# Kernel tuning notes

Measured on AMD Instinct MI355X. Metric: run time of the kernel, lower is better.

The kernel has to match this reference:

```python
import jax, jax.numpy as jnp
import numpy as np

N = 50000
E = 250000
IN = 256
H = 4
D = 64  # h_feats // n_heads
C = 153


def setup_inputs() -> dict:
    key = jax.random.key(0)
    ks = jax.random.split(key, 32)
    def nrm(k, shape, scale=0.05):
        return jax.random.normal(k, shape, dtype=jnp.float32) * scale
    inp = {
        'x': nrm(ks[0], (N, IN), 1.0),
        'edge_index_a': jax.random.randint(ks[1], (2, E), 0, N, dtype=jnp.int32),
        'edge_index_b': jax.random.randint(ks[2], (2, E), 0, N, dtype=jnp.int32),
    }
    i = 3
    for layer in (0, 1):
        for et in ('a', 'b'):
            inp[f'W{layer}{et}'] = nrm(ks[i], (IN if layer == 0 else H * D, H * D)); i += 1
            inp[f'asrc{layer}{et}'] = nrm(ks[i], (H, D)); i += 1
            inp[f'adst{layer}{et}'] = nrm(ks[i], (H, D)); i += 1
            inp[f'b{layer}{et}'] = nrm(ks[i], (H * D,)); i += 1
    inp['Wout'] = nrm(ks[i], (H * D, C)); i += 1
    inp['bout'] = nrm(ks[i], (C,))
    return inp


def gat_conv(x, edge_index, W, a_src, a_dst, b):
    # PyG GATConv: shared linear, per-edge attention, dst-segmented softmax
    h = (x @ W).reshape(N, H, D)                 # [N, H, D]
    s_src = jnp.sum(h * a_src, axis=-1)          # [N, H]
    s_dst = jnp.sum(h * a_dst, axis=-1)          # [N, H]
    src, dst = edge_index[0], edge_index[1]
    e = jax.nn.leaky_relu(s_src[src] + s_dst[dst], negative_slope=0.2)  # [E, H]
    m = jax.ops.segment_max(e, dst, num_segments=N)                     # [N, H]
    m = jnp.where(jnp.isfinite(m), m, 0.0)       # isolated nodes -> 0
    p = jnp.exp(e - m[dst])                      # [E, H]
    z = jax.ops.segment_sum(p, dst, num_segments=N)
    alpha = p / (z[dst] + 1e-16)                 # [E, H]
    out = jax.ops.segment_sum(h[src] * alpha[:, :, None], dst, num_segments=N)
    return out.reshape(N, H * D) + b


def reference(x, edge_index_a, edge_index_b,
              W0a, asrc0a, adst0a, b0a, W0b, asrc0b, adst0b, b0b,
              W1a, asrc1a, adst1a, b1a, W1b, asrc1b, adst1b, b1b,
              Wout, bout):
    # layer 0: HeteroConv sums outputs of per-etype GATConvs
    h = gat_conv(x, edge_index_a, W0a, asrc0a, adst0a, b0a) + \
        gat_conv(x, edge_index_b, W0b, asrc0b, adst0b, b0b)
    h = jax.nn.leaky_relu(h, negative_slope=0.01)  # F.leaky_relu default; dropout is identity in eval
    # layer 1 (no activation after last layer)
    h = gat_conv(h, edge_index_a, W1a, asrc1a, adst1a, b1a) + \
        gat_conv(h, edge_index_b, W1b, asrc1b, adst1b, b1b)
    return h @ Wout + bout
```

## Files before the change

kernel.cpp:

```cpp
#include <hip/hip_runtime.h>
#include <math.h>

#define N_NODES 50000
#define E_EDGES 250000
#define HD 256
#define NH 4
#define DH 64
#define NC 153
#define KDIM 256
#define HD2 512
#define SLOTS 64

__device__ __forceinline__ unsigned short f2bf(float f) {
    unsigned u = __float_as_uint(f);
    u = u + 0x7FFFu + ((u >> 16) & 1u);
    return (unsigned short)(u >> 16);
}
__device__ __forceinline__ float bf2f(unsigned short b) {
    return __uint_as_float(((unsigned)b) << 16);
}

typedef __attribute__((ext_vector_type(8))) short bf16x8;
typedef __attribute__((ext_vector_type(4))) float f32x4;

template<int NCB, bool SCORES>
__global__ __launch_bounds__(256, 4) void gemm_k256(
        const unsigned short* __restrict__ A, const unsigned short* __restrict__ BT,
        float* __restrict__ Cf, unsigned short* __restrict__ Cbf,
        const float* __restrict__ bias,
        const float* __restrict__ as_a, const float* __restrict__ ad_a,
        const float* __restrict__ as_b, const float* __restrict__ ad_b,
        float* __restrict__ ssrc8, float* __restrict__ sdst8,
        int M, int Ncols) {
    __shared__ unsigned short Bs[64 * 256];
    const int tid = threadIdx.x;
    const int lane = tid & 63;
    const int wave = tid >> 6;
    const int quad = lane >> 4;
    const int l16 = lane & 15;

    const int nwg = gridDim.x;
    const int wg = blockIdx.x;
    const int x = wg & 7, ii = wg >> 3;
    const int q = nwg >> 3, r = nwg & 7;
    const int logical = (x < r ? x * (q + 1) : r * (q + 1) + (x - r) * q) + ii;
    const int cb = logical % NCB;
    const int rb = logical / NCB;
    const int row0 = rb * 128 + wave * 32;
    const int col0 = cb * 64;

    #pragma unroll
    for (int j = 0; j < 8; j++) {
        const int c = tid + 256 * j;
        const int rr = c >> 5;
        const int kb = (c & 31) << 4;
        const uint4 v = *(const uint4*)((const char*)BT +
                            (size_t)(col0 + rr) * 512 + kb);
        *(uint4*)((char*)Bs + rr * 512 + (kb ^ ((rr & 7) << 4))) = v;
    }
    __syncthreads();

    f32x4 acc[2][4];
    #pragma unroll
    for (int i = 0; i < 2; i++)
        #pragma unroll
        for (int j = 0; j < 4; j++) acc[i][j] = (f32x4)0.f;

    size_t a_off[2];
    #pragma unroll
    for (int mt = 0; mt < 2; mt++) {
        int gr = row0 + mt * 16 + l16;
        if (gr >= M) gr = M - 1;
        a_off[mt] = (size_t)gr * KDIM + quad * 8;
    }
    const char* Bsc = (const char*)Bs;
    const int bbase = l16 * 512 + ((quad * 16) ^ ((l16 & 7) << 4));

    bf16x8 a_buf[4][2];
    bf16x8 b_cur[4], b_nxt[4];
    #pragma unroll
    for (int s = 0; s < 3; s++)
        #pragma unroll
        for (int mt = 0; mt < 2; mt++)
            a_buf[s][mt] = *(const bf16x8*)&A[a_off[mt] + s * 32];
    #pragma unroll
    for (int nt = 0; nt < 4; nt++)
        b_cur[nt] = *(const bf16x8*)(Bsc + nt * 16 * 512 + bbase);

    #pragma unroll
    for (int kk = 0; kk < 8; kk++) {
        if (kk + 3 < 8) {
            #pragma unroll
            for (int mt = 0; mt < 2; mt++)
                a_buf[(kk + 3) & 3][mt] =
                    *(const bf16x8*)&A[a_off[mt] + (kk + 3) * 32];
        }
        if (kk < 7) {
            #pragma unroll
            for (int nt = 0; nt < 4; nt++)
                b_nxt[nt] = *(const bf16x8*)(Bsc + nt * 16 * 512 +
                                (bbase ^ ((kk + 1) * 64)));
        }
        #pragma unroll
        for (int mt = 0; mt < 2; mt++)
            #pragma unroll
            for (int nt = 0; nt < 4; nt++)
                acc[mt][nt] = __builtin_amdgcn_mfma_f32_16x16x32_bf16(
                                  a_buf[kk & 3][mt], b_cur[nt], acc[mt][nt], 0, 0, 0);
        #pragma unroll
        for (int nt = 0; nt < 4; nt++) b_cur[nt] = b_nxt[nt];
    }

    if constexpr (SCORES) {
        const float* as_p = (cb < 4) ? as_a : as_b;
        const float* ad_p = (cb < 4) ? ad_a : ad_b;
        const int hd = (cb & 3) * 64;
        float asv[4], adv[4];
        #pragma unroll
        for (int nt = 0; nt < 4; nt++) {
            asv[nt] = as_p[hd + nt * 16 + l16];
            adv[nt] = ad_p[hd + nt * 16 + l16];
        }
        #pragma unroll
        for (int mt = 0; mt < 2; mt++) {
            #pragma unroll
            for (int rr = 0; rr < 4; rr++) {
                float ps = acc[mt][0][rr] * asv[0] + acc[mt][1][rr] * asv[1]
                         + acc[mt][2][rr] * asv[2] + acc[mt][3][rr] * asv[3];
                float pd = acc[mt][0][rr] * adv[0] + acc[mt][1][rr] * adv[1]
                         + acc[mt][2][rr] * adv[2] + acc[mt][3][rr] * adv[3];
                #pragma unroll
                for (int off = 1; off < 16; off <<= 1) {
                    ps += __shfl_xor(ps, off);
                    pd += __shfl_xor(pd, off);
                }
                const int m = row0 + mt * 16 + quad * 4 + rr;
                if (l16 == 0 && m < M) {
                    ssrc8[m * 8 + cb] = ps;
                    sdst8[m * 8 + cb] = pd;
                }
            }
        }

        __syncthreads();
        char* myC = (char*)Bs + wave * 4096;
        #pragma unroll
        for (int mt = 0; mt < 2; mt++)
            #pragma unroll
            for (int nt = 0; nt < 4; nt++)
                #pragma unroll
                for (int rr = 0; rr < 4; rr++)
                    *(unsigned short*)(myC + (mt * 16 + quad * 4 + rr) * 128 +
                                       (nt * 16 + l16) * 2) = f2bf(acc[mt][nt][rr]);
        #pragma unroll
        for (int it = 0; it < 4; it++) {
            const int chunk = it * 64 + lane;
            const int lr = chunk >> 3;
            const int cbyte = (chunk & 7) * 16;
            const uint4 v = *(const uint4*)(myC + lr * 128 + cbyte);
            const int m = row0 + lr;
            if (m < M)
                *(uint4*)((char*)Cbf + ((size_t)m * Ncols + col0) * 2 + cbyte) = v;
        }
    } else {
        #pragma unroll
        for (int mt = 0; mt < 2; mt++) {
            #pragma unroll
            for (int nt = 0; nt < 4; nt++) {
                const int n = col0 + nt * 16 + l16;
                if (n >= Ncols) continue;
                const float bv = bias ? bias[n] : 0.f;
                #pragma unroll
                for (int rr = 0; rr < 4; rr++) {
                    const int m = row0 + mt * 16 + quad * 4 + rr;
                    if (m < M) Cf[(size_t)m * Ncols + n] = acc[mt][nt][rr] + bv;
                }
            }
        }
    }
}

__global__ __launch_bounds__(256) void convert_bf16_kernel(
        const float* __restrict__ in, unsigned short* __restrict__ out, int n) {
    const int i = (blockIdx.x * 256 + threadIdx.x) * 4;
    if (i + 3 < n) {
        const float4 v = *(const float4*)&in[i];
        ushort4 o;
        o.x = f2bf(v.x); o.y = f2bf(v.y); o.z = f2bf(v.z); o.w = f2bf(v.w);
        *(ushort4*)&out[i] = o;
    } else {
        for (int j = i; j < n; j++) out[j] = f2bf(in[j]);
    }
}

__global__ __launch_bounds__(256) void wt2_kernel(
        const float* __restrict__ Wa, const float* __restrict__ Wb,
        unsigned short* __restrict__ Wt) {
    const int idx = blockIdx.x * 256 + threadIdx.x;
    const int n = idx >> 8, k = idx & 255;
    Wt[idx] = (n < HD) ? f2bf(Wa[(size_t)k * HD + n])
                       : f2bf(Wb[(size_t)k * HD + (n - HD)]);
}

__global__ __launch_bounds__(256) void wt_kernel(
        const float* __restrict__ W, unsigned short* __restrict__ Wt, int Nc) {
    const int idx = blockIdx.x * 256 + threadIdx.x;
    const int n = idx >> 8, k = idx & 255;
    Wt[idx] = (n < Nc) ? f2bf(W[(size_t)k * Nc + n]) : (unsigned short)0;
}

__global__ __launch_bounds__(256) void zero_int_kernel(int* __restrict__ p, int n) {
    const int i = blockIdx.x * 256 + threadIdx.x;
    if (i < n) p[i] = 0;
}

__global__ __launch_bounds__(256) void hist2_kernel(
        const int* __restrict__ ei_a, const int* __restrict__ ei_b,
        int* __restrict__ deg) {
    const int t = blockIdx.x * 256 + threadIdx.x;
    if (t < E_EDGES)          atomicAdd(&deg[ei_a[E_EDGES + t]], 1);
    else if (t < 2 * E_EDGES) atomicAdd(&deg[N_NODES + ei_b[t]], 1);
}

__global__ __launch_bounds__(1024) void scan_local_kernel(
        const int* __restrict__ deg, int* __restrict__ excl,
        int* __restrict__ bsums, int n) {
    __shared__ int wsum[16];
    const int i = blockIdx.x * 1024 + threadIdx.x;
    const int lane = threadIdx.x & 63;
    const int wid = threadIdx.x >> 6;
    const int v = (i < n) ? deg[i] : 0;
    int s = v;
    #pragma unroll
    for (int off = 1; off < 64; off <<= 1) {
        const int t = __shfl_up(s, off);
        if (lane >= off) s += t;
    }
    if (lane == 63) wsum[wid] = s;
    __syncthreads();
    if (wid == 0) {
        int wv = (lane < 16) ? wsum[lane] : 0;
        #pragma unroll
        for (int off = 1; off < 16; off <<= 1) {
            const int t = __shfl_up(wv, off);
            if (lane >= off) wv += t;
        }
        if (lane < 16) wsum[lane] = wv;
    }
    __syncthreads();
    const int woff = (wid > 0) ? wsum[wid - 1] : 0;
    if (i < n) excl[i] = s - v + woff;
    if (threadIdx.x == 1023) bsums[blockIdx.x] = wsum[15];
}

__global__ __launch_bounds__(64) void scan_bsums_kernel(
        int* __restrict__ bsums, int nb) {
    const int lane = threadIdx.x;
    const int b0 = (lane < nb) ? bsums[lane] : 0;
    const int b1 = (64 + lane < nb) ? bsums[64 + lane] : 0;
    int s0 = b0, s1 = b1;
    #pragma unroll
    for (int off = 1; off < 64; off <<= 1) {
        const int t0 = __shfl_up(s0, off);
        const int t1 = __shfl_up(s1, off);
        if (lane >= off) { s0 += t0; s1 += t1; }
    }
    const int tot0 = __shfl(s0, 63);
    bsums[lane] = s0 - b0;
    bsums[64 + lane] = tot0 + s1 - b1;
}

__global__ __launch_bounds__(256) void scan_add2_kernel(
        const int* __restrict__ excl, const int* __restrict__ bsums,
        int* __restrict__ rp_a, int* __restrict__ rp_b,
        int* __restrict__ cursor, int n2) {
    const int i = blockIdx.x * 256 + threadIdx.x;
    if (i >= n2) return;
    const int v = excl[i] + bsums[i >> 10];
    if (i < N_NODES) { rp_a[i] = v; cursor[i] = v; }
    else { const int w = v - E_EDGES; rp_b[i - N_NODES] = w; cursor[i] = w; }
    if (i == 0) { rp_a[N_NODES] = E_EDGES; rp_b[N_NODES] = E_EDGES; }
}

__global__ __launch_bounds__(256) void scatter2_kernel(
        const int* __restrict__ ei_a, const int* __restrict__ ei_b,
        int* __restrict__ cursor,
        int* __restrict__ cs_a, int* __restrict__ cs_b) {
    const int t = blockIdx.x * 256 + threadIdx.x;
    if (t < E_EDGES) {
        const int src = ei_a[t], dst = ei_a[E_EDGES + t];
        cs_a[atomicAdd(&cursor[dst], 1)] = src;
    } else if (t < 2 * E_EDGES) {
        const int src = ei_b[t - E_EDGES], dst = ei_b[t];
        cs_b[atomicAdd(&cursor[N_NODES + dst], 1)] = src;
    }
}

__global__ __launch_bounds__(256) void aggregate_both_kernel(
        const int* __restrict__ rp_a, const int* __restrict__ cs_a,
        const int* __restrict__ rp_b, const int* __restrict__ cs_b,
        const unsigned short* __restrict__ h_ab,
        const float* __restrict__ ssrc8, const float* __restrict__ sdst8,
        const float* __restrict__ b1, const float* __restrict__ b2,
        unsigned short* __restrict__ out_bf, int do_leaky) {
    __shared__ float s_lds[4][2][NH][SLOTS];
    __shared__ int   src_lds[4][2][SLOTS];
    const int wv = threadIdx.x >> 6;
    const int node = blockIdx.x * 4 + wv;
    const int lane = threadIdx.x & 63;
    if (node >= N_NODES) return;
    const int hh = lane >> 4;
    const int l16 = lane & 15;
    const int c4 = lane * 4;

    float4 a = make_float4(0.f, 0.f, 0.f, 0.f);

    #pragma unroll
    for (int et = 0; et < 2; et++) {
        const int* rp = et ? rp_b : rp_a;
        const int* cs = et ? cs_b : cs_a;
        const size_t hoff = et ? (size_t)HD : 0;
        const int r8 = et * 4 + hh;
        const float sdv = sdst8[node * 8 + r8];
        const int beg = rp[node], end = rp[node + 1];
        float* sld = &s_lds[wv][et][hh][0];
        int*   srl = &src_lds[wv][et][0];

        float mm = -INFINITY;
        for (int c = beg; c < end; c += 16) {
            const int e = c + l16;
            float s = -INFINITY;
            if (e < end) {
                const int srci = cs[e];
                s = ssrc8[srci * 8 + r8] + sdv;
                s = (s >= 0.f) ? s : 0.2f * s;
                const int sl = e - beg;
                if (sl < SLOTS) {
                    sld[sl] = s;
                    if (hh == 0) srl[sl] = srci;
                }
            }
            #pragma unroll
            for (int off = 1; off < 16; off <<= 1)
                s = fmaxf(s, __shfl_xor(s, off));
            mm = fmaxf(mm, s);
        }

        float4 t = make_float4(0.f, 0.f, 0.f, 0.f);
        float z = 0.f;
        int e = beg;
        for (; e + 3 < end; e += 4) {
            const int sl = e - beg;
            int s0, s1, s2, s3;
            float p0, p1, p2, p3;
            if (sl + 3 < SLOTS) {
                const int4 sv = *(const int4*)&srl[sl];
                s0 = sv.x; s1 = sv.y; s2 = sv.z; s3 = sv.w;
                const float4 sc = *(const float4*)&sld[sl];
                p0 = __expf(sc.x - mm);
                p1 = __expf(sc.y - mm);
                p2 = __expf(sc.z - mm);
                p3 = __expf(sc.w - mm);
            } else {
                s0 = cs[e + 0]; s1 = cs[e + 1]; s2 = cs[e + 2]; s3 = cs[e + 3];
                float v0 = ssrc8[s0 * 8 + r8] + sdv; v0 = (v0 >= 0.f) ? v0 : 0.2f * v0;
                float v1 = ssrc8[s1 * 8 + r8] + sdv; v1 = (v1 >= 0.f) ? v1 : 0.2f * v1;
                float v2 = ssrc8[s2 * 8 + r8] + sdv; v2 = (v2 >= 0.f) ? v2 : 0.2f * v2;
                float v3 = ssrc8[s3 * 8 + r8] + sdv; v3 = (v3 >= 0.f) ? v3 : 0.2f * v3;
                p0 = __expf(v0 - mm);
                p1 = __expf(v1 - mm);
                p2 = __expf(v2 - mm);
                p3 = __expf(v3 - mm);
            }
            z += (p0 + p1) + (p2 + p3);
            const ushort4 h0 = *(const ushort4*)&h_ab[(size_t)s0 * HD2 + hoff + c4];
            const ushort4 h1 = *(const ushort4*)&h_ab[(size_t)s1 * HD2 + hoff + c4];
            const ushort4 h2 = *(const ushort4*)&h_ab[(size_t)s2 * HD2 + hoff + c4];
            const ushort4 h3 = *(const ushort4*)&h_ab[(size_t)s3 * HD2 + hoff + c4];
            t.x = fmaf(p0, bf2f(h0.x), t.x); t.y = fmaf(p0, bf2f(h0.y), t.y);
            t.z = fmaf(p0, bf2f(h0.z), t.z); t.w = fmaf(p0, bf2f(h0.w), t.w);
            t.x = fmaf(p1, bf2f(h1.x), t.x); t.y = fmaf(p1, bf2f(h1.y), t.y);
            t.z = fmaf(p1, bf2f(h1.z), t.z); t.w = fmaf(p1, bf2f(h1.w), t.w);
            t.x = fmaf(p2, bf2f(h2.x), t.x); t.y = fmaf(p2, bf2f(h2.y), t.y);
            t.z = fmaf(p2, bf2f(h2.z), t.z); t.w = fmaf(p2, bf2f(h2.w), t.w);
            t.x = fmaf(p3, bf2f(h3.x), t.x); t.y = fmaf(p3, bf2f(h3.y), t.y);
            t.z = fmaf(p3, bf2f(h3.z), t.z); t.w = fmaf(p3, bf2f(h3.w), t.w);
        }
        for (; e < end; e++) {
            const int sl = e - beg;
            int src; float p;
            if (sl < SLOTS) {
                src = srl[sl];
                p = __expf(sld[sl] - mm);
            } else {
                src = cs[e];
                float v0 = ssrc8[src * 8 + r8] + sdv; v0 = (v0 >= 0.f) ? v0 : 0.2f * v0;
                p = __expf(v0 - mm);
            }
            z += p;
            const ushort4 hv = *(const ushort4*)&h_ab[(size_t)src * HD2 + hoff + c4];
            t.x = fmaf(p, bf2f(hv.x), t.x);
            t.y = fmaf(p, bf2f(hv.y), t.y);
            t.z = fmaf(p, bf2f(hv.z), t.z);
            t.w = fmaf(p, bf2f(hv.w), t.w);
        }

        const float zz = 1.f / (z + 1e-16f);
        a.x = fmaf(t.x, zz, a.x);
        a.y = fmaf(t.y, zz, a.y);
        a.z = fmaf(t.z, zz, a.z);
        a.w = fmaf(t.w, zz, a.w);
    }

    const float4 bv1 = *(const float4*)&b1[c4];
    const float4 bv2 = *(const float4*)&b2[c4];
    float4 v;
    v.x = a.x + bv1.x + bv2.x;
    v.y = a.y + bv1.y + bv2.y;
    v.z = a.z + bv1.z + bv2.z;
    v.w = a.w + bv1.w + bv2.w;
    if (do_leaky) {
        v.x = (v.x >= 0.f) ? v.x : 0.01f * v.x;
        v.y = (v.y >= 0.f) ? v.y : 0.01f * v.y;
        v.z = (v.z >= 0.f) ? v.z : 0.01f * v.z;
        v.w = (v.w >= 0.f) ? v.w : 0.01f * v.w;
    }
    ushort4 o;
    o.x = f2bf(v.x); o.y = f2bf(v.y); o.z = f2bf(v.z); o.w = f2bf(v.w);
    *(ushort4*)&out_bf[(size_t)node * HD + c4] = o;
}

#define N_ROWBLK128 ((N_NODES + 127) / 128)

static void run_layer(const unsigned short* a_bf,
                      const int* rp_a, const int* cs_a,
                      const int* rp_b, const int* cs_b,
                      const float* Wa, const float* Wb,
                      const float* as_a, const float* ad_a,
                      const float* as_b, const float* ad_b,
                      const float* b1, const float* b2,
                      unsigned short* Wt2, unsigned short* h_ab,
                      float* ssrc8, float* sdst8,
                      unsigned short* out_bf, int do_leaky,
                      hipStream_t stream) {
    wt2_kernel<<<HD2, 256, 0, stream>>>(Wa, Wb, Wt2);
    gemm_k256<8, true><<<N_ROWBLK128 * 8, 256, 0, stream>>>(
        a_bf, Wt2, nullptr, h_ab, nullptr,
        as_a, ad_a, as_b, ad_b, ssrc8, sdst8, N_NODES, HD2);
    aggregate_both_kernel<<<(N_NODES + 3) / 4, 256, 0, stream>>>(
        rp_a, cs_a, rp_b, cs_b, h_ab, ssrc8, sdst8,
        b1, b2, out_bf, do_leaky);
}

extern "C" void kernel_launch(void* const* d_in, const int* in_sizes, int n_in,
                              void* d_out, int out_size, void* d_ws, size_t ws_size,
                              hipStream_t stream) {
    const float* x    = (const float*)d_in[0];
    const int*   ei_a = (const int*)d_in[1];
    const int*   ei_b = (const int*)d_in[2];
    const float* W0a = (const float*)d_in[3];
    const float* as0a = (const float*)d_in[4];
    const float* ad0a = (const float*)d_in[5];
    const float* b0a = (const float*)d_in[6];
    const float* W0b = (const float*)d_in[7];
    const float* as0b = (const float*)d_in[8];
    const float* ad0b = (const float*)d_in[9];
    const float* b0b = (const float*)d_in[10];
    const float* W1a = (const float*)d_in[11];
    const float* as1a = (const float*)d_in[12];
    const float* ad1a = (const float*)d_in[13];
    const float* b1a = (const float*)d_in[14];
    const float* W1b = (const float*)d_in[15];
    const float* as1b = (const float*)d_in[16];
    const float* ad1b = (const float*)d_in[17];
    const float* b1b = (const float*)d_in[18];
    const float* Wout = (const float*)d_in[19];
    const float* bout = (const float*)d_in[20];
    float* out = (float*)d_out;

    unsigned short* h_ab  = (unsigned short*)d_ws;
    unsigned short* bf_in = h_ab + (size_t)N_NODES * HD2;
    unsigned short* Wt2   = bf_in + (size_t)N_NODES * HD;
    float* ssrc8  = (float*)(Wt2 + (size_t)HD2 * KDIM);
    float* sdst8  = ssrc8 + (size_t)N_NODES * 8;
    int*   ibase  = (int*)(sdst8 + (size_t)N_NODES * 8);
    int* deg     = ibase;
    int* cursor  = deg + 2 * N_NODES;
    int* rp_a    = cursor + 2 * N_NODES;
    int* cs_a    = rp_a + N_NODES + 1;
    int* rp_b    = cs_a + E_EDGES;
    int* cs_b    = rp_b + N_NODES + 1;
    int* excl    = cs_b + E_EDGES;
    int* bsums   = excl + 2 * N_NODES;

    const size_t NF = (size_t)N_NODES * HD;
    const int nf4_blocks = (int)((NF / 4 + 255) / 256);
    const int n2 = 2 * N_NODES;
    const int sb = (n2 + 1023) / 1024;

    zero_int_kernel<<<(n2 + 255) / 256, 256, 0, stream>>>(deg, n2);
    hist2_kernel<<<(2 * E_EDGES + 255) / 256, 256, 0, stream>>>(ei_a, ei_b, deg);
    scan_local_kernel<<<sb, 1024, 0, stream>>>(deg, excl, bsums, n2);
    scan_bsums_kernel<<<1, 64, 0, stream>>>(bsums, sb);
    scan_add2_kernel<<<(n2 + 255) / 256, 256, 0, stream>>>(
        excl, bsums, rp_a, rp_b, cursor, n2);
    scatter2_kernel<<<(2 * E_EDGES + 255) / 256, 256, 0, stream>>>(
        ei_a, ei_b, cursor, cs_a, cs_b);

    convert_bf16_kernel<<<nf4_blocks, 256, 0, stream>>>(x, bf_in, (int)NF);
    run_layer(bf_in, rp_a, cs_a, rp_b, cs_b, W0a, W0b,
              as0a, ad0a, as0b, ad0b, b0a, b0b, Wt2, h_ab,
              ssrc8, sdst8, bf_in, 1, stream);

    run_layer(bf_in, rp_a, cs_a, rp_b, cs_b, W1a, W1b,
              as1a, ad1a, as1b, ad1b, b1a, b1b, Wt2, h_ab,
              ssrc8, sdst8, bf_in, 0, stream);

    wt_kernel<<<KDIM, 256, 0, stream>>>(Wout, Wt2, NC);
    gemm_k256<3, false><<<N_ROWBLK128 * 3, 256, 0, stream>>>(
        bf_in, Wt2, out, nullptr, bout,
        nullptr, nullptr, nullptr, nullptr, nullptr, nullptr, N_NODES, NC);
}
```

Baseline: 401.9 us.

## Fuse CSR build into one cooperative kernel and merge aggregate tail loop

Replaces the six separate CSR-construction launches (zero, histogram, two-level scan, add, scatter) with a single cooperative kernel of 512 blocks that uses grid-wide syncs between phases, removing per-launch overhead and inter-kernel gaps. The scan now works on 256-element chunks with a single-wave carry scan over block sums. The aggregation loop also folds its scalar remainder into the 4-wide body using masks, which pads to four gathers with zero weights. Grid syncs add their own latency, and the masked path performs redundant loads for short tails.

```diff
diff --git a/kernel.cpp b/kernel.cpp
--- a/kernel.cpp
+++ b/kernel.cpp
@@ -1,5 +1,8 @@
 #include <hip/hip_runtime.h>
+#include <hip/hip_cooperative_groups.h>
 #include <math.h>
+
+namespace cg = cooperative_groups;
 
 #define N_NODES 50000
 #define E_EDGES 250000
@@ -10,6 +13,7 @@
 #define KDIM 256
 #define HD2 512
 #define SLOTS 64
+#define CSR_GRID 512
 
 __device__ __forceinline__ unsigned short f2bf(float f) {
     unsigned u = __float_as_uint(f);
@@ -209,90 +213,85 @@
     Wt[idx] = (n < Nc) ? f2bf(W[(size_t)k * Nc + n]) : (unsigned short)0;
 }
 
-__global__ __launch_bounds__(256) void zero_int_kernel(int* __restrict__ p, int n) {
-    const int i = blockIdx.x * 256 + threadIdx.x;
-    if (i < n) p[i] = 0;
-}
-
-__global__ __launch_bounds__(256) void hist2_kernel(
+__global__ __launch_bounds__(256) void csr_build_coop(
         const int* __restrict__ ei_a, const int* __restrict__ ei_b,
-        int* __restrict__ deg) {
-    const int t = blockIdx.x * 256 + threadIdx.x;
-    if (t < E_EDGES)          atomicAdd(&deg[ei_a[E_EDGES + t]], 1);
-    else if (t < 2 * E_EDGES) atomicAdd(&deg[N_NODES + ei_b[t]], 1);
-}
-
-__global__ __launch_bounds__(1024) void scan_local_kernel(
-        const int* __restrict__ deg, int* __restrict__ excl,
-        int* __restrict__ bsums, int n) {
-    __shared__ int wsum[16];
-    const int i = blockIdx.x * 1024 + threadIdx.x;
+        int* __restrict__ deg, int* __restrict__ cursor,
+        int* __restrict__ rp_a, int* __restrict__ cs_a,
+        int* __restrict__ rp_b, int* __restrict__ cs_b,
+        int* __restrict__ excl, int* __restrict__ bsums) {
+    cg::grid_group grid = cg::this_grid();
+    const int nt = gridDim.x * 256;
+    const int gt = blockIdx.x * 256 + threadIdx.x;
     const int lane = threadIdx.x & 63;
-    const int wid = threadIdx.x >> 6;
-    const int v = (i < n) ? deg[i] : 0;
-    int s = v;
-    #pragma unroll
-    for (int off = 1; off < 64; off <<= 1) {
-        const int t = __shfl_up(s, off);
-        if (lane >= off) s += t;
-    }
-    if (lane == 63) wsum[wid] = s;
-    __syncthreads();
-    if (wid == 0) {
-        int wv = (lane < 16) ? wsum[lane] : 0;
-        #pragma unroll
-        for (int off = 1; off < 16; off <<= 1) {
-            const int t = __shfl_up(wv, off);
-            if (lane >= off) wv += t;
-        }
-        if (lane < 16) wsum[lane] = wv;
-    }
-    __syncthreads();
-    const int woff = (wid > 0) ? wsum[wid - 1] : 0;
-    if (i < n) excl[i] = s - v + woff;
-    if (threadIdx.x == 1023) bsums[blockIdx.x] = wsum[15];
-}
-
-__global__ __launch_bounds__(64) void scan_bsums_kernel(
-        int* __restrict__ bsums, int nb) {
-    const int lane = threadIdx.x;
-    const int b0 = (lane < nb) ? bsums[lane] : 0;
-    const int b1 = (64 + lane < nb) ? bsums[64 + lane] : 0;
-    int s0 = b0, s1 = b1;
-    #pragma unroll
-    for (int off = 1; off < 64; off <<= 1) {
-        const int t0 = __shfl_up(s0, off);
-        const int t1 = __shfl_up(s1, off);
-        if (lane >= off) { s0 += t0; s1 += t1; }
-    }
-    const int tot0 = __shfl(s0, 63);
-    bsums[lane] = s0 - b0;
-    bsums[64 + lane] = tot0 + s1 - b1;
-}
-
-__global__ __launch_bounds__(256) void scan_add2_kernel(
-        const int* __restrict__ excl, const int* __restrict__ bsums,
-        int* __restrict__ rp_a, int* __restrict__ rp_b,
-        int* __restrict__ cursor, int n2) {
-    const int i = blockIdx.x * 256 + threadIdx.x;
-    if (i >= n2) return;
-    const int v = excl[i] + bsums[i >> 10];
-    if (i < N_NODES) { rp_a[i] = v; cursor[i] = v; }
-    else { const int w = v - E_EDGES; rp_b[i - N_NODES] = w; cursor[i] = w; }
-    if (i == 0) { rp_a[N_NODES] = E_EDGES; rp_b[N_NODES] = E_EDGES; }
-}
-
-__global__ __launch_bounds__(256) void scatter2_kernel(
-        const int* __restrict__ ei_a, const int* __restrict__ ei_b,
-        int* __restrict__ cursor,
-        int* __restrict__ cs_a, int* __restrict__ cs_b) {
-    const int t = blockIdx.x * 256 + threadIdx.x;
-    if (t < E_EDGES) {
-        const int src = ei_a[t], dst = ei_a[E_EDGES + t];
-        cs_a[atomicAdd(&cursor[dst], 1)] = src;
-    } else if (t < 2 * E_EDGES) {
-        const int src = ei_b[t - E_EDGES], dst = ei_b[t];
-        cs_b[atomicAdd(&cursor[N_NODES + dst], 1)] = src;
+    const int wid  = threadIdx.x >> 6;
+    const int n2 = 2 * N_NODES;
+    const int e2 = 2 * E_EDGES;
+    const int nchunks = (n2 + 255) / 256;
+
+    for (int i = gt; i < n2; i += nt) deg[i] = 0;
+    grid.sync();
+
+    for (int t = gt; t < e2; t += nt) {
+        if (t < E_EDGES) atomicAdd(&deg[ei_a[E_EDGES + t]], 1);
+        else             atomicAdd(&deg[N_NODES + ei_b[t]], 1);
+    }
+    grid.sync();
+
+    __shared__ int wsum[4];
+    for (int c = blockIdx.x; c < nchunks; c += gridDim.x) {
+        const int i = c * 256 + threadIdx.x;
+        const int v = (i < n2) ? deg[i] : 0;
+        int s = v;
+        #pragma unroll
+        for (int off = 1; off < 64; off <<= 1) {
+            const int t = __shfl_up(s, off);
+            if (lane >= off) s += t;
+        }
+        if (lane == 63) wsum[wid] = s;
+        __syncthreads();
+        int woff = 0;
+        #pragma unroll
+        for (int w = 0; w < 3; w++) if (w < wid) woff += wsum[w];
+        if (i < n2) excl[i] = s - v + woff;
+        if (threadIdx.x == 0)
+            bsums[c] = wsum[0] + wsum[1] + wsum[2] + wsum[3];
+        __syncthreads();
+    }
+    grid.sync();
+
+    if (blockIdx.x == 0 && threadIdx.x < 64) {
+        int carry = 0;
+        for (int base = 0; base < nchunks; base += 64) {
+            const int idx = base + lane;
+            const int v = (idx < nchunks) ? bsums[idx] : 0;
+            int s = v;
+            #pragma unroll
+            for (int off = 1; off < 64; off <<= 1) {
+                const int t = __shfl_up(s, off);
+                if (lane >= off) s += t;
+            }
+            if (idx < nchunks) bsums[idx] = carry + s - v;
+            carry += __shfl(s, 63);
+        }
+    }
+    grid.sync();
+
+    for (int i = gt; i < n2; i += nt) {
+        const int v = excl[i] + bsums[i >> 8];
+        if (i < N_NODES) { rp_a[i] = v; cursor[i] = v; }
+        else { const int w = v - E_EDGES; rp_b[i - N_NODES] = w; cursor[i] = w; }
+    }
+    if (gt == 0) { rp_a[N_NODES] = E_EDGES; rp_b[N_NODES] = E_EDGES; }
+    grid.sync();
+
+    for (int t = gt; t < e2; t += nt) {
+        if (t < E_EDGES) {
+            const int src = ei_a[t], dst = ei_a[E_EDGES + t];
+            cs_a[atomicAdd(&cursor[dst], 1)] = src;
+        } else {
+            const int src = ei_b[t - E_EDGES], dst = ei_b[t];
+            cs_b[atomicAdd(&cursor[N_NODES + dst], 1)] = src;
+        }
     }
 }
 
@@ -348,61 +347,51 @@
 
         float4 t = make_float4(0.f, 0.f, 0.f, 0.f);
         float z = 0.f;
-        int e = beg;
-        for (; e + 3 < end; e += 4) {
-            const int sl = e - beg;
-            int s0, s1, s2, s3;
-            float p0, p1, p2, p3;
+        for (int e0 = beg; e0 < end; e0 += 4) {
+            const int sl = e0 - beg;
             if (sl + 3 < SLOTS) {
+                const bool m1 = (e0 + 1 < end);
+                const bool m2 = (e0 + 2 < end);
+                const bool m3 = (e0 + 3 < end);
                 const int4 sv = *(const int4*)&srl[sl];
-                s0 = sv.x; s1 = sv.y; s2 = sv.z; s3 = sv.w;
                 const float4 sc = *(const float4*)&sld[sl];
-                p0 = __expf(sc.x - mm);
-                p1 = __expf(sc.y - mm);
-                p2 = __expf(sc.z - mm);
-                p3 = __expf(sc.w - mm);
+                const int s0 = sv.x;
+                const int s1 = m1 ? sv.y : s0;
+                const int s2 = m2 ? sv.z : s0;
+                const int s3 = m3 ? sv.w : s0;
+                const float p0 = __expf(sc.x - mm);
+                const float p1 = m1 ? __expf(sc.y - mm) : 0.f;
+                const float p2 = m2 ? __expf(sc.z - mm) : 0.f;
+                const float p3 = m3 ? __expf(sc.w - mm) : 0.f;
+                z += (p0 + p1) + (p2 + p3);
+                const ushort4 h0 = *(const ushort4*)&h_ab[(size_t)s0 * HD2 + hoff + c4];
+                const ushort4 h1 = *(const ushort4*)&h_ab[(size_t)s1 * HD2 + hoff + c4];
+                const ushort4 h2 = *(const ushort4*)&h_ab[(size_t)s2 * HD2 + hoff + c4];
+                const ushort4 h3 = *(const ushort4*)&h_ab[(size_t)s3 * HD2 + hoff + c4];
+                t.x = fmaf(p0, bf2f(h0.x), t.x); t.y = fmaf(p0, bf2f(h0.y), t.y);
+                t.z = fmaf(p0, bf2f(h0.z), t.z); t.w = fmaf(p0, bf2f(h0.w), t.w);
+                t.x = fmaf(p1, bf2f(h1.x), t.x); t.y = fmaf(p1, bf2f(h1.y), t.y);
+                t.z = fmaf(p1, bf2f(h1.z), t.z); t.w = fmaf(p1, bf2f(h1.w), t.w);
+                t.x = fmaf(p2, bf2f(h2.x), t.x); t.y = fmaf(p2, bf2f(h2.y), t.y);
+                t.z = fmaf(p2, bf2f(h2.z), t.z); t.w = fmaf(p2, bf2f(h2.w), t.w);
+                t.x = fmaf(p3, bf2f(h3.x), t.x); t.y = fmaf(p3, bf2f(h3.y), t.y);
+                t.z = fmaf(p3, bf2f(h3.z), t.z); t.w = fmaf(p3, bf2f(h3.w), t.w);
             } else {
-                s0 = cs[e + 0]; s1 = cs[e + 1]; s2 = cs[e + 2]; s3 = cs[e + 3];
-                float v0 = ssrc8[s0 * 8 + r8] + sdv; v0 = (v0 >= 0.f) ? v0 : 0.2f * v0;
-                float v1 = ssrc8[s1 * 8 + r8] + sdv; v1 = (v1 >= 0.f) ? v1 : 0.2f * v1;
-                float v2 = ssrc8[s2 * 8 + r8] + sdv; v2 = (v2 >= 0.f) ? v2 : 0.2f * v2;
-                float v3 = ssrc8[s3 * 8 + r8] + sdv; v3 = (v3 >= 0.f) ? v3 : 0.2f * v3;
-                p0 = __expf(v0 - mm);
-                p1 = __expf(v1 - mm);
-                p2 = __expf(v2 - mm);
-                p3 = __expf(v3 - mm);
+                const int eend = (e0 + 4 < end) ? e0 + 4 : end;
+                for (int e = e0; e < eend; e++) {
+                    const int src = cs[e];
+                    float v0 = ssrc8[src * 8 + r8] + sdv;
+                    v0 = (v0 >= 0.f) ? v0 : 0.2f * v0;
+                    const float p = __expf(v0 - mm);
+                    z += p;
+                    const ushort4 hv =
+                        *(const ushort4*)&h_ab[(size_t)src * HD2 + hoff + c4];
+                    t.x = fmaf(p, bf2f(hv.x), t.x);
+                    t.y = fmaf(p, bf2f(hv.y), t.y);
+                    t.z = fmaf(p, bf2f(hv.z), t.z);
+                    t.w = fmaf(p, bf2f(hv.w), t.w);
+                }
             }
-            z += (p0 + p1) + (p2 + p3);
-            const ushort4 h0 = *(const ushort4*)&h_ab[(size_t)s0 * HD2 + hoff + c4];
-            const ushort4 h1 = *(const ushort4*)&h_ab[(size_t)s1 * HD2 + hoff + c4];
-            const ushort4 h2 = *(const ushort4*)&h_ab[(size_t)s2 * HD2 + hoff + c4];
-            const ushort4 h3 = *(const ushort4*)&h_ab[(size_t)s3 * HD2 + hoff + c4];
-            t.x = fmaf(p0, bf2f(h0.x), t.x); t.y = fmaf(p0, bf2f(h0.y), t.y);
-            t.z = fmaf(p0, bf2f(h0.z), t.z); t.w = fmaf(p0, bf2f(h0.w), t.w);
-            t.x = fmaf(p1, bf2f(h1.x), t.x); t.y = fmaf(p1, bf2f(h1.y), t.y);
-            t.z = fmaf(p1, bf2f(h1.z), t.z); t.w = fmaf(p1, bf2f(h1.w), t.w);
-            t.x = fmaf(p2, bf2f(h2.x), t.x); t.y = fmaf(p2, bf2f(h2.y), t.y);
-            t.z = fmaf(p2, bf2f(h2.z), t.z); t.w = fmaf(p2, bf2f(h2.w), t.w);
-            t.x = fmaf(p3, bf2f(h3.x), t.x); t.y = fmaf(p3, bf2f(h3.y), t.y);
-            t.z = fmaf(p3, bf2f(h3.z), t.z); t.w = fmaf(p3, bf2f(h3.w), t.w);
-        }
-        for (; e < end; e++) {
-            const int sl = e - beg;
-            int src; float p;
-            if (sl < SLOTS) {
-                src = srl[sl];
-                p = __expf(sld[sl] - mm);
-            } else {
-                src = cs[e];
-                float v0 = ssrc8[src * 8 + r8] + sdv; v0 = (v0 >= 0.f) ? v0 : 0.2f * v0;
-                p = __expf(v0 - mm);
-            }
-            z += p;
-            const ushort4 hv = *(const ushort4*)&h_ab[(size_t)src * HD2 + hoff + c4];
-            t.x = fmaf(p, bf2f(hv.x), t.x);
-            t.y = fmaf(p, bf2f(hv.y), t.y);
-            t.z = fmaf(p, bf2f(hv.z), t.z);
-            t.w = fmaf(p, bf2f(hv.w), t.w);
         }
 
         const float zz = 1.f / (z + 1e-16f);
@@ -495,17 +484,16 @@
 
     const size_t NF = (size_t)N_NODES * HD;
     const int nf4_blocks = (int)((NF / 4 + 255) / 256);
-    const int n2 = 2 * N_NODES;
-    const int sb = (n2 + 1023) / 1024;
-
-    zero_int_kernel<<<(n2 + 255) / 256, 256, 0, stream>>>(deg, n2);
-    hist2_kernel<<<(2 * E_EDGES + 255) / 256, 256, 0, stream>>>(ei_a, ei_b, deg);
-    scan_local_kernel<<<sb, 1024, 0, stream>>>(deg, excl, bsums, n2);
-    scan_bsums_kernel<<<1, 64, 0, stream>>>(bsums, sb);
-    scan_add2_kernel<<<(n2 + 255) / 256, 256, 0, stream>>>(
-        excl, bsums, rp_a, rp_b, cursor, n2);
-    scatter2_kernel<<<(2 * E_EDGES + 255) / 256, 256, 0, stream>>>(
-        ei_a, ei_b, cursor, cs_a, cs_b);
+
+    {
+        void* args[] = {
+            (void*)&ei_a, (void*)&ei_b, (void*)&deg, (void*)&cursor,
+            (void*)&rp_a, (void*)&cs_a, (void*)&rp_b, (void*)&cs_b,
+            (void*)&excl, (void*)&bsums
+        };
+        hipLaunchCooperativeKernel((const void*)csr_build_coop,
+                                   dim3(CSR_GRID), dim3(256), args, 0, stream);
+    }
 
     convert_bf16_kernel<<<nf4_blocks, 256, 0, stream>>>(x, bf_in, (int)NF);
     run_layer(bf_in, rp_a, cs_a, rp_b, cs_b, W0a, W0b,
```

After: 688.7 us. 71.4% more time.
